# Kernel tuning notes

Hardware: AMD Instinct MI355X
Metric: run time of the kernel (lower is better)

Reference implementation:

```python
import math
import jax, jax.numpy as jnp
import numpy as np

N_LAYER = 4
D = 192        # n_embd
NH = 4         # n_head
N = 3072       # n_neurons = n_embd * mlp_dim_mult // n_head
VOCAB = 256
BLOCK = 4096
EPS = 1e-5
B, T = 1, 1024


def get_freqs(n, theta=2.0 ** 16):
    t = np.arange(n, dtype=np.float32)
    q = np.floor(t / 2.0) * 2.0  # quantize(t, 2)
    return (1.0 / theta ** (q / n) / (2.0 * math.pi)).astype(np.float32)

_FREQS = jnp.asarray(get_freqs(N))  # [N]


def _ln(x):
    # LayerNorm over last dim, no affine (elementwise_affine=False)
    m = jnp.mean(x, axis=-1, keepdims=True)
    v = jnp.var(x, axis=-1, keepdims=True)
    return (x - m) / jnp.sqrt(v + EPS)


def _rope(x):
    # x: [B, nh, T, N]
    t = x.shape[2]
    phases = (jnp.arange(t, dtype=jnp.float32)[:, None] * _FREQS[None, :]) % 1.0 * (2.0 * math.pi)  # [T, N]
    x_even = x[..., 0::2]
    x_odd = x[..., 1::2]
    v_rot = jnp.stack((-x_odd, x_even), axis=-1).reshape(x.shape)
    return x * jnp.cos(phases) + v_rot * jnp.sin(phases)


def setup_inputs() -> dict:
    key = jax.random.key(0)
    ks = jax.random.split(key, 7)
    s = 0.02
    return {
        "idx": jax.random.randint(ks[0], (B, T), 0, VOCAB, dtype=jnp.int64)
        if jax.config.jax_enable_x64 else jax.random.randint(ks[0], (B, T), 0, VOCAB, dtype=jnp.int32),
        "decoder_x": jax.random.normal(ks[1], (NH, D, N), jnp.float32) * s,
        "decoder_y": jax.random.normal(ks[2], (NH, D, N), jnp.float32) * s,
        "encoder": jax.random.normal(ks[3], (NH * N, D), jnp.float32) * s,
        "embed": jax.random.normal(ks[4], (VOCAB, D), jnp.float32) * s,
        "pos_emb": jax.random.normal(ks[5], (BLOCK, D), jnp.float32) * s,
        "lm_head": jax.random.normal(ks[6], (D, VOCAB), jnp.float32) * s,
    }


def reference(idx, decoder_x, decoder_y, encoder, embed, pos_emb, lm_head):
    b, t = idx.shape
    x = embed[idx] + pos_emb[:t][None]          # [B, T, D]
    x = _ln(x)
    mask = jnp.tril(jnp.ones((t, t), jnp.float32), k=-1)  # strictly lower
    for _ in range(N_LAYER):
        # encoder-side sparsification: D -> N per head
        x_sparse = jax.nn.relu(jnp.einsum('btd,hdn->bhtn', x, decoder_x))  # [B,nh,T,N]
        qr = _rope(x_sparse)
        scores = jnp.einsum('bhtn,bhsn->bhts', qr, qr) * mask              # [B,nh,T,T]
        ykv = _ln(jnp.einsum('bhts,bsd->bhtd', scores, x))                 # [B,nh,T,D]
        y_sparse = jax.nn.relu(jnp.einsum('bhtd,hdn->bhtn', ykv, decoder_y))
        xy = x_sparse * y_sparse                                           # [B,nh,T,N]
        # [B,T,nh*N] @ [nh*N, D]
        ymlp = jnp.einsum('bhtn,hnd->btd', xy, encoder.reshape(NH, N, D))
        x = _ln(x + _ln(ymlp))
    logits = jnp.einsum('btd,dv->btv', x, lm_head)                         # [B,T,vocab]
    return logits
```

## Files before the change

kernel.cpp:

```cpp
#include <hip/hip_runtime.h>
#include <hip/hip_bf16.h>

using bf16 = __hip_bfloat16;

#define D_DIM   192
#define N_DIM   3072
#define NHEAD   4
#define T_SEQ   1024
#define HN      12288
#define NP2     1536
#define VOCABSZ 256
#define NLAYER  4
#define LN_EPS  1e-5f
#define TWO_PI  6.2831853071795864f

typedef __attribute__((ext_vector_type(8)))  short          s16x8;
typedef __attribute__((ext_vector_type(8)))  unsigned short u16x8;
typedef __attribute__((ext_vector_type(4)))  float          f32x4;
typedef __attribute__((ext_vector_type(16))) float          f32x16;

__device__ __forceinline__ float b2f(bf16 v) { return __bfloat162float(v); }
__device__ __forceinline__ float us2f(unsigned short u) {
    unsigned int x = ((unsigned int)u) << 16;
    return __builtin_bit_cast(float, x);
}
__device__ __forceinline__ unsigned short f2us(float f) {
    bf16 b = __float2bfloat16(f);
    return __builtin_bit_cast(unsigned short, b);
}

__global__ void fill_out(float* __restrict__ out, float val, int nelem) {
    int i = blockIdx.x * 256 + threadIdx.x;
    if (i < nelem) out[i] = val;
}

__global__ void t_cvt(const float* __restrict__ in, bf16* __restrict__ out,
                      int R, int C, long inZ, long outZ) {
    __shared__ float tile[64][65];
    in  += inZ  * blockIdx.z;
    out += outZ * blockIdx.z;
    const int tx = threadIdx.x & 63, ty = threadIdx.x >> 6;
    const int r0 = blockIdx.y * 64, c0 = blockIdx.x * 64;
    #pragma unroll
    for (int rr = 0; rr < 16; rr++) {
        int row = ty * 16 + rr;
        tile[row][tx] = in[(size_t)(r0 + row) * C + c0 + tx];
    }
    __syncthreads();
    #pragma unroll
    for (int rr = 0; rr < 16; rr++) {
        int row = ty * 16 + rr;
        out[(size_t)(c0 + row) * R + r0 + tx] = __float2bfloat16(tile[tx][row]);
    }
}

__device__ __forceinline__ void wave_sum2(float& s, float& ss) {
    #pragma unroll
    for (int off = 1; off < 64; off <<= 1) {
        s  += __shfl_xor(s,  off, 64);
        ss += __shfl_xor(ss, off, 64);
    }
}

__global__ void k_embed(const int* __restrict__ idx, const float* __restrict__ emb,
                        const float* __restrict__ pos, float* __restrict__ x) {
    int t = blockIdx.x, l = threadIdx.x;
    int tok = idx[t];
    const float* e = emb + tok * D_DIM;
    const float* p = pos + t * D_DIM;
    float v0 = e[l] + p[l], v1 = e[l + 64] + p[l + 64], v2 = e[l + 128] + p[l + 128];
    float s = v0 + v1 + v2, ss = v0 * v0 + v1 * v1 + v2 * v2;
    wave_sum2(s, ss);
    float m = s / D_DIM, r = rsqrtf(ss / D_DIM - m * m + LN_EPS);
    float* xr = x + t * D_DIM;
    xr[l] = (v0 - m) * r; xr[l + 64] = (v1 - m) * r; xr[l + 128] = (v2 - m) * r;
}

__global__ void k_ln(float* __restrict__ buf) {
    int l = threadIdx.x;
    float* row = buf + (size_t)blockIdx.x * D_DIM;
    float v0 = row[l], v1 = row[l + 64], v2 = row[l + 128];
    float s = v0 + v1 + v2, ss = v0 * v0 + v1 * v1 + v2 * v2;
    wave_sum2(s, ss);
    float m = s / D_DIM, r = rsqrtf(ss / D_DIM - m * m + LN_EPS);
    row[l] = (v0 - m) * r; row[l + 64] = (v1 - m) * r; row[l + 128] = (v2 - m) * r;
}

__global__ void k_ln2(float* __restrict__ buf, const float* __restrict__ P1) {
    int l = threadIdx.x;
    size_t off = (size_t)blockIdx.x * D_DIM;
    float* row = buf + off;
    const float* r1 = P1 + off;
    float v0 = row[l] + r1[l];
    float v1 = row[l + 64] + r1[l + 64];
    float v2 = row[l + 128] + r1[l + 128];
    float s = v0 + v1 + v2, ss = v0 * v0 + v1 * v1 + v2 * v2;
    wave_sum2(s, ss);
    float m = s / D_DIM, r = rsqrtf(ss / D_DIM - m * m + LN_EPS);
    row[l] = (v0 - m) * r; row[l + 64] = (v1 - m) * r; row[l + 128] = (v2 - m) * r;
}

__global__ void k_resid8(float* __restrict__ x, const float* __restrict__ P) {
    int l = threadIdx.x, t = blockIdx.x;
    float y0 = 0.f, y1 = 0.f, y2 = 0.f;
    #pragma unroll
    for (int p = 0; p < 8; p++) {
        const float* r = P + (size_t)p * T_SEQ * D_DIM + (size_t)t * D_DIM;
        y0 += r[l]; y1 += r[l + 64]; y2 += r[l + 128];
    }
    float* xr = x + (size_t)t * D_DIM;
    float s = y0 + y1 + y2, ss = y0 * y0 + y1 * y1 + y2 * y2;
    wave_sum2(s, ss);
    float m1 = s / D_DIM, r1 = rsqrtf(ss / D_DIM - m1 * m1 + LN_EPS);
    float v0 = xr[l] + (y0 - m1) * r1;
    float v1 = xr[l + 64] + (y1 - m1) * r1;
    float v2 = xr[l + 128] + (y2 - m1) * r1;
    s = v0 + v1 + v2; ss = v0 * v0 + v1 * v1 + v2 * v2;
    wave_sum2(s, ss);
    float m2 = s / D_DIM, r2 = rsqrtf(ss / D_DIM - m2 * m2 + LN_EPS);
    xr[l] = (v0 - m2) * r2; xr[l + 64] = (v1 - m2) * r2; xr[l + 128] = (v2 - m2) * r2;
}

__global__ void k_tables(ushort2* __restrict__ csT) {
    int gid = blockIdx.x * 256 + threadIdx.x;
    int t = gid / NP2, p = gid % NP2;
    float qf = (float)(2 * p);
    float f = exp2f(qf * (-16.0f / 3072.0f)) * (1.0f / (float)TWO_PI);
    float ph = fmodf((float)t * f, 1.0f) * (float)TWO_PI;
    ushort2 cs;
    cs.x = f2us(cosf(ph));
    cs.y = f2us(sinf(ph));
    csT[gid] = cs;
}

__launch_bounds__(256, 4)
__global__ void scores64(const bf16* __restrict__ qr, bf16* __restrict__ sc,
                         bf16* __restrict__ dbuf) {
    const int h  = blockIdx.z;
    const int kh = blockIdx.y;
    const int orig = blockIdx.x;
    const int L = (orig & 7) * 17 + (orig >> 3);
    int i = 0;
    while (((i + 1) * (i + 2)) >> 1 <= L) ++i;
    int j = L - ((i * (i + 1)) >> 1);
    const int t0 = i * 64, s0 = j * 64;
    const bool diag = (i == j);

    int arow = t0, brow = s0;
    if (kh == 1 && !diag) { arow = s0; brow = t0; }

    __shared__ short As[2][64][72];
    __shared__ short Bs[2][64][72];

    const int tid = threadIdx.x;
    const int lane = tid & 63, w = tid >> 6;
    const int wtm = (w >> 1) * 32, wtn = (w & 1) * 32;
    const int l31 = lane & 31, lhi = lane >> 5;
    const int r0 = tid >> 2;
    const int kq = (tid & 3) * 16;

    const int kBeg = kh * (N_DIM / 2);
    const bf16* gA = qr + (size_t)(arow + r0) * HN + h * N_DIM + kBeg + kq;
    const bf16* gB = qr + (size_t)(brow + r0) * HN + h * N_DIM + kBeg + kq;

    u16x8 pa0, pa1, pb0, pb1;
    u16x8 qa0, qa1, qb0, qb1;
    auto load0 = [&](int k0) {
        pa0 = *(const u16x8*)(gA + k0);
        pa1 = *(const u16x8*)(gA + k0 + 8);
        pb0 = *(const u16x8*)(gB + k0);
        pb1 = *(const u16x8*)(gB + k0 + 8);
    };
    auto load1 = [&](int k0) {
        qa0 = *(const u16x8*)(gA + k0);
        qa1 = *(const u16x8*)(gA + k0 + 8);
        qb0 = *(const u16x8*)(gB + k0);
        qb1 = *(const u16x8*)(gB + k0 + 8);
    };
    auto dep0 = [&](int buf) {
        *(u16x8*)&As[buf][r0][kq]     = pa0;
        *(u16x8*)&As[buf][r0][kq + 8] = pa1;
        *(u16x8*)&Bs[buf][r0][kq]     = pb0;
        *(u16x8*)&Bs[buf][r0][kq + 8] = pb1;
    };
    auto dep1 = [&](int buf) {
        *(u16x8*)&As[buf][r0][kq]     = qa0;
        *(u16x8*)&As[buf][r0][kq + 8] = qa1;
        *(u16x8*)&Bs[buf][r0][kq]     = qb0;
        *(u16x8*)&Bs[buf][r0][kq + 8] = qb1;
    };

    f32x16 acc;
    #pragma unroll
    for (int r = 0; r < 16; r++) acc[r] = 0.f;

    auto mfma_step = [&](int buf) {
        #pragma unroll
        for (int ks = 0; ks < 4; ks++) {
            s16x8 a = *(const s16x8*)&As[buf][wtm + l31][ks * 16 + lhi * 8];
            s16x8 b = *(const s16x8*)&Bs[buf][wtn + l31][ks * 16 + lhi * 8];
            acc = __builtin_amdgcn_mfma_f32_32x32x16_bf16(a, b, acc, 0, 0, 0);
        }
    };

    const int NIT = (N_DIM / 2) / 64;
    load0(0);
    load1(64);
    dep0(0);
    __syncthreads();

    for (int k = 0; k < NIT; k += 2) {
        if (k + 2 < NIT) load0((k + 2) * 64);
        mfma_step(0);
        if (k + 1 < NIT) dep1(1);
        __syncthreads();
        if (k + 1 < NIT) {
            if (k + 3 < NIT) load1((k + 3) * 64);
            mfma_step(1);
            if (k + 2 < NIT) dep0(0);
            __syncthreads();
        }
    }

    __syncthreads();
    short (*S)[72] = (short(*)[72])&As[0][0][0];
    #pragma unroll
    for (int r = 0; r < 16; r++) {
        int row = wtm + (r & 3) + 8 * (r >> 2) + 4 * lhi;
        int col = wtn + l31;
        float v = acc[r];
        if (diag && col >= row) v = 0.f;
        S[row][col] = (short)f2us(v);
    }
    __syncthreads();
    if (kh == 1 && diag) {
        bf16* P = dbuf + (size_t)(h * 16 + i) * 4096;
        #pragma unroll
        for (int e = 0; e < 2; e++) {
            int idxe = tid + e * 256;
            int row = idxe >> 3, cg = (idxe & 7) * 8;
            u16x8 v = *(const u16x8*)&S[row][cg];
            *(u16x8*)(P + row * 64 + cg) = v;
        }
    } else {
        bf16* C = sc + (size_t)h * T_SEQ * T_SEQ;
        #pragma unroll
        for (int e = 0; e < 2; e++) {
            int idxe = tid + e * 256;
            int row = idxe >> 3, cg = (idxe & 7) * 8;
            u16x8 v = *(const u16x8*)&S[row][cg];
            *(u16x8*)(C + (size_t)(arow + row) * T_SEQ + brow + cg) = v;
        }
    }
}

__global__ void k_comb(bf16* __restrict__ sc, const bf16* __restrict__ dbuf) {
    __shared__ short tile[64][72];
    const int h = blockIdx.z;
    int L = blockIdx.x;
    int i = 0;
    while (((i + 1) * (i + 2)) >> 1 <= L) ++i;
    int j = L - ((i * (i + 1)) >> 1);
    bf16* C = sc + (size_t)h * T_SEQ * T_SEQ;
    const int r  = threadIdx.x >> 3;
    const int c8 = (threadIdx.x & 7) * 8;
    if (i != j) {
        #pragma unroll
        for (int p = 0; p < 2; p++) {
            int row = r + p * 32;
            u16x8 v = *(const u16x8*)(C + (size_t)(j * 64 + row) * T_SEQ + i * 64 + c8);
            *(u16x8*)&tile[row][c8] = v;
        }
        __syncthreads();
        #pragma unroll
        for (int p = 0; p < 2; p++) {
            int row = r + p * 32;
            size_t off = (size_t)(i * 64 + row) * T_SEQ + j * 64 + c8;
            u16x8 a = *(const u16x8*)(C + off);
            u16x8 o;
            #pragma unroll
            for (int e = 0; e < 8; e++)
                o[e] = f2us(us2f(a[e]) + us2f((unsigned short)tile[c8 + e][row]));
            *(u16x8*)(C + off) = o;
        }
    } else {
        const bf16* P = dbuf + (size_t)(h * 16 + i) * 4096;
        #pragma unroll
        for (int p = 0; p < 2; p++) {
            int row = r + p * 32;
            size_t off = (size_t)(i * 64 + row) * T_SEQ + i * 64 + c8;
            u16x8 a = *(const u16x8*)(C + off);
            u16x8 b = *(const u16x8*)((const unsigned short*)P + row * 64 + c8);
            u16x8 o;
            #pragma unroll
            for (int e = 0; e < 8; e++)
                o[e] = f2us(us2f(a[e]) + us2f(b[e]));
            *(u16x8*)(C + off) = o;
        }
    }
}

__device__ __forceinline__ void stage_rope8(short* dst, const bf16* src,
                                            const ushort2* csP) {
    u16x8 v  = *(const u16x8*)src;
    u16x8 cs = *(const u16x8*)csP;
    u16x8 o;
    #pragma unroll
    for (int i = 0; i < 4; i++) {
        float e  = us2f(v[2 * i]), od = us2f(v[2 * i + 1]);
        float c  = us2f(cs[2 * i]), s = us2f(cs[2 * i + 1]);
        o[2 * i]     = f2us(e * c - od * s);
        o[2 * i + 1] = f2us(od * c + e * s);
    }
    *(u16x8*)dst = o;
}

__launch_bounds__(256)
__global__ void scores_fused(const bf16* __restrict__ xs,
                             const ushort2* __restrict__ csT,
                             bf16* __restrict__ sc) {
    const int h  = blockIdx.z;
    const int s0 = blockIdx.x * 64, t0 = blockIdx.y * 64;
    if (s0 > t0) return;
    __shared__ short As[64][40];
    __shared__ short Bs[64][40];
    const int tid  = threadIdx.x;
    const int srow = tid >> 2, kq = (tid & 3) * 8;
    const int lane = tid & 63, w = tid >> 6, qd = lane >> 4, lc = lane & 15;
    const int tA = t0 + srow, tB = s0 + srow;
    const bf16* gA = xs + (size_t)tA * HN + h * N_DIM + kq;
    const bf16* gB = xs + (size_t)tB * HN + h * N_DIM + kq;
    const ushort2* cA = csT + (size_t)tA * NP2 + (kq >> 1);
    const ushort2* cB = csT + (size_t)tB * NP2 + (kq >> 1);
    f32x4 acc[4] = {{0.f,0.f,0.f,0.f},{0.f,0.f,0.f,0.f},
                    {0.f,0.f,0.f,0.f},{0.f,0.f,0.f,0.f}};
    for (int k0 = 0; k0 < N_DIM; k0 += 32) {
        stage_rope8(&As[srow][kq], gA + k0, cA + (k0 >> 1));
        stage_rope8(&Bs[srow][kq], gB + k0, cB + (k0 >> 1));
        __syncthreads();
        s16x8 a = *(const s16x8*)&As[w * 16 + lc][qd * 8];
        #pragma unroll
        for (int j = 0; j < 4; j++) {
            s16x8 b = *(const s16x8*)&Bs[j * 16 + lc][qd * 8];
            acc[j] = __builtin_amdgcn_mfma_f32_16x16x32_bf16(a, b, acc[j], 0, 0, 0);
        }
        __syncthreads();
    }
    bf16* C = sc + (size_t)h * T_SEQ * T_SEQ;
    const bool diag = (s0 == t0);
    const int tbase = t0 + w * 16 + qd * 4;
    #pragma unroll
    for (int j = 0; j < 4; j++) {
        int s = s0 + j * 16 + lc;
        #pragma unroll
        for (int r = 0; r < 4; r++) {
            int t = tbase + r;
            C[(size_t)t * T_SEQ + s] =
                __float2bfloat16((!diag || s < t) ? acc[j][r] : 0.f);
        }
    }
}

template <int EPI, bool WQR>
__launch_bounds__(256)
__global__ void dgemm128(const float* __restrict__ A, const bf16* __restrict__ Bt,
                         bf16* __restrict__ xs, bf16* __restrict__ qr,
                         const ushort2* __restrict__ csT) {
    __shared__ __align__(16) short pool[2 * 2 * 128 * 40];
    short (*As)[128][40] = (short(*)[128][40])pool;
    short (*Bs)[128][40] = (short(*)[128][40])(pool + 2 * 128 * 40);

    const int tid = threadIdx.x;
    const int lane = tid & 63, w = tid >> 6, qd = lane >> 4, lc = lane & 15;
    const int wtm = (w >> 1) * 64, wtn = (w & 1) * 64;
    const int n0 = blockIdx.x * 128, m0 = blockIdx.y * 128;
    if constexpr (EPI == 2) A += (size_t)(n0 / N_DIM) * T_SEQ * D_DIM;

    const int r0 = tid >> 2, r1 = r0 + 64;
    const int kq = (tid & 3) * 8;

    const float* gA = A  + kq;
    const bf16*  gB = Bt + kq;

    float4 fa00, fa01, fa02, fa03, fa10, fa11, fa12, fa13;
    u16x8 pb00, pb01, pb10, pb11;
    auto load0 = [&](int k0) {
        const float* a0 = gA + (size_t)(m0 + r0) * D_DIM + k0;
        const float* a1 = gA + (size_t)(m0 + r1) * D_DIM + k0;
        fa00 = *(const float4*)a0; fa01 = *(const float4*)(a0 + 4);
        fa02 = *(const float4*)a1; fa03 = *(const float4*)(a1 + 4);
        pb00 = *(const u16x8*)(gB + (size_t)(n0 + r0) * D_DIM + k0);
        pb01 = *(const u16x8*)(gB + (size_t)(n0 + r1) * D_DIM + k0);
    };
    auto load1 = [&](int k0) {
        const float* a0 = gA + (size_t)(m0 + r0) * D_DIM + k0;
        const float* a1 = gA + (size_t)(m0 + r1) * D_DIM + k0;
        fa10 = *(const float4*)a0; fa11 = *(const float4*)(a0 + 4);
        fa12 = *(const float4*)a1; fa13 = *(const float4*)(a1 + 4);
        pb10 = *(const u16x8*)(gB + (size_t)(n0 + r0) * D_DIM + k0);
        pb11 = *(const u16x8*)(gB + (size_t)(n0 + r1) * D_DIM + k0);
    };
    auto dep0 = [&](int buf) {
        u16x8 o0, o1;
        o0[0] = f2us(fa00.x); o0[1] = f2us(fa00.y); o0[2] = f2us(fa00.z); o0[3] = f2us(fa00.w);
        o0[4] = f2us(fa01.x); o0[5] = f2us(fa01.y); o0[6] = f2us(fa01.z); o0[7] = f2us(fa01.w);
        o1[0] = f2us(fa02.x); o1[1] = f2us(fa02.y); o1[2] = f2us(fa02.z); o1[3] = f2us(fa02.w);
        o1[4] = f2us(fa03.x); o1[5] = f2us(fa03.y); o1[6] = f2us(fa03.z); o1[7] = f2us(fa03.w);
        *(u16x8*)&As[buf][r0][kq] = o0;
        *(u16x8*)&As[buf][r1][kq] = o1;
        *(u16x8*)&Bs[buf][r0][kq] = pb00;
        *(u16x8*)&Bs[buf][r1][kq] = pb01;
    };
    auto dep1 = [&](int buf) {
        u16x8 o0, o1;
        o0[0] = f2us(fa10.x); o0[1] = f2us(fa10.y); o0[2] = f2us(fa10.z); o0[3] = f2us(fa10.w);
        o0[4] = f2us(fa11.x); o0[5] = f2us(fa11.y); o0[6] = f2us(fa11.z); o0[7] = f2us(fa11.w);
        o1[0] = f2us(fa12.x); o1[1] = f2us(fa12.y); o1[2] = f2us(fa12.z); o1[3] = f2us(fa12.w);
        o1[4] = f2us(fa13.x); o1[5] = f2us(fa13.y); o1[6] = f2us(fa13.z); o1[7] = f2us(fa13.w);
        *(u16x8*)&As[buf][r0][kq] = o0;
        *(u16x8*)&As[buf][r1][kq] = o1;
        *(u16x8*)&Bs[buf][r0][kq] = pb10;
        *(u16x8*)&Bs[buf][r1][kq] = pb11;
    };

    f32x4 acc[4][4] = {};
    auto mfma_step = [&](int buf) {
        s16x8 a[4], b[4];
        #pragma unroll
        for (int m = 0; m < 4; m++) a[m] = *(const s16x8*)&As[buf][wtm + m * 16 + lc][qd * 8];
        #pragma unroll
        for (int n = 0; n < 4; n++) b[n] = *(const s16x8*)&Bs[buf][wtn + n * 16 + lc][qd * 8];
        #pragma unroll
        for (int m = 0; m < 4; m++)
            #pragma unroll
            for (int n = 0; n < 4; n++)
                acc[m][n] = __builtin_amdgcn_mfma_f32_16x16x32_bf16(a[m], b[n], acc[m][n], 0, 0, 0);
    };

    const int NIT = D_DIM / 32;
    load0(0);
    load1(32);
    dep0(0);
    __syncthreads();
    for (int k = 0; k < NIT; k += 2) {
        if (k + 2 < NIT) load0((k + 2) * 32);
        mfma_step(0);
        if (k + 1 < NIT) dep1(1);
        __syncthreads();
        if (k + 1 < NIT) {
            if (k + 3 < NIT) load1((k + 3) * 32);
            mfma_step(1);
            if (k + 2 < NIT) dep0(0);
            __syncthreads();
        }
    }

    short (*S)[136] = (short(*)[136])pool;
    #pragma unroll
    for (int m = 0; m < 4; m++) {
        #pragma unroll
        for (int r = 0; r < 4; r++) {
            int tl = wtm + m * 16 + qd * 4 + r;
            #pragma unroll
            for (int n = 0; n < 4; n++) {
                int cl = wtn + n * 16 + lc;
                S[tl][cl] = (short)f2us(fmaxf(acc[m][n][r], 0.f));
            }
        }
    }
    __syncthreads();
    #pragma unroll
    for (int e = 0; e < 8; e++) {
        int idxe = tid + e * 256;
        int row = idxe >> 4, cg = idxe & 15;
        u16x8 v = *(const u16x8*)&S[row][cg * 8];
        int t = m0 + row, ngg = n0 + cg * 8;
        size_t ci = (size_t)t * HN + ngg;
        if constexpr (EPI == 1) {
            *(u16x8*)(xs + ci) = v;
            if constexpr (WQR) {
                int p0 = (ngg % N_DIM) >> 1;
                u16x8 cs8 = *(const u16x8*)&csT[(size_t)t * NP2 + p0];
                u16x8 o;
                #pragma unroll
                for (int q = 0; q < 4; q++) {
                    float ev = us2f(v[2 * q]), ov = us2f(v[2 * q + 1]);
                    float c = us2f(cs8[2 * q]), s = us2f(cs8[2 * q + 1]);
                    o[2 * q]     = f2us(ev * c - ov * s);
                    o[2 * q + 1] = f2us(ov * c + ev * s);
                }
                *(u16x8*)(qr + ci) = o;
            }
        } else {
            u16x8 g = *(const u16x8*)(xs + ci);
            u16x8 o;
            #pragma unroll
            for (int q = 0; q < 8; q++) o[q] = f2us(us2f(g[q]) * us2f(v[q]));
            *(u16x8*)(xs + ci) = o;
        }
    }
}

template <typename TA, int MODE>
__launch_bounds__(256)
__global__ void mfma_gemm(const TA* __restrict__ A, const bf16* __restrict__ Bt,
                          float* __restrict__ C,
                          int K, int kSeg, int lda, int ldb, int ldc,
                          long aZ, long bZ, long cZ) {
    __shared__ short As[2][64][72];
    __shared__ short Bs[2][64][72];

    const int z = blockIdx.z;
    const int tid = threadIdx.x;
    const int n0 = blockIdx.x * 64, m0 = blockIdx.y * 64;
    const int srow = tid >> 2, sk = (tid & 3) * 16;
    const int lane = tid & 63, w = tid >> 6, qd = lane >> 4, lc = lane & 15;

    int kBeg, kEnd;
    if constexpr (MODE == 1) {
        const int h = z >> 1, seg = z & 1;
        A += aZ * h;
        C += cZ * h + bZ * seg;
        const int kc = (m0 + 64 < K) ? m0 + 64 : K;
        const int half0 = ((kc + 127) >> 7) << 6;
        kBeg = seg ? half0 : 0;
        kEnd = seg ? kc : half0;
    } else if constexpr (MODE == 2) {
        A += aZ * z; Bt += bZ * z; C += cZ * z;
        kBeg = z * kSeg; kEnd = kBeg + kSeg;
    } else if constexpr (MODE == 3) {
        A += aZ * z; Bt += bZ * z; C += cZ * z;
        kBeg = 0; kEnd = (m0 + 64 < K) ? m0 + 64 : K;
    } else {
        A += aZ * z; Bt += bZ * z; C += cZ * z;
        kBeg = 0; kEnd = K;
    }

    const TA*   ga = A  + (size_t)(m0 + srow) * lda + sk;
    const bf16* gb = Bt + (size_t)(n0 + srow) * ldb + sk;

    float4 f00, f01, f02, f03, f10, f11, f12, f13;
    u16x8 pa00, pa01, pa10, pa11, pb00, pb01, pb10, pb11;
    auto load0 = [&](int k0) {
        if constexpr (__is_same(TA, float)) {
            f00 = *(const float4*)(ga + k0);
            f01 = *(const float4*)(ga + k0 + 4);
            f02 = *(const float4*)(ga + k0 + 8);
            f03 = *(const float4*)(ga + k0 + 12);
        } else {
            pa00 = *(const u16x8*)(ga + k0);
            pa01 = *(const u16x8*)(ga + k0 + 8);
        }
        pb00 = *(const u16x8*)(gb + k0);
        pb01 = *(const u16x8*)(gb + k0 + 8);
    };
    auto load1 = [&](int k0) {
        if constexpr (__is_same(TA, float)) {
            f10 = *(const float4*)(ga + k0);
            f11 = *(const float4*)(ga + k0 + 4);
            f12 = *(const float4*)(ga + k0 + 8);
            f13 = *(const float4*)(ga + k0 + 12);
        } else {
            pa10 = *(const u16x8*)(ga + k0);
            pa11 = *(const u16x8*)(ga + k0 + 8);
        }
        pb10 = *(const u16x8*)(gb + k0);
        pb11 = *(const u16x8*)(gb + k0 + 8);
    };
    auto dep0 = [&](int buf) {
        if constexpr (__is_same(TA, float)) {
            u16x8 o0, o1;
            o0[0] = f2us(f00.x); o0[1] = f2us(f00.y); o0[2] = f2us(f00.z); o0[3] = f2us(f00.w);
            o0[4] = f2us(f01.x); o0[5] = f2us(f01.y); o0[6] = f2us(f01.z); o0[7] = f2us(f01.w);
            o1[0] = f2us(f02.x); o1[1] = f2us(f02.y); o1[2] = f2us(f02.z); o1[3] = f2us(f02.w);
            o1[4] = f2us(f03.x); o1[5] = f2us(f03.y); o1[6] = f2us(f03.z); o1[7] = f2us(f03.w);
            *(u16x8*)&As[buf][srow][sk]     = o0;
            *(u16x8*)&As[buf][srow][sk + 8] = o1;
        } else {
            *(u16x8*)&As[buf][srow][sk]     = pa00;
            *(u16x8*)&As[buf][srow][sk + 8] = pa01;
        }
        *(u16x8*)&Bs[buf][srow][sk]     = pb00;
        *(u16x8*)&Bs[buf][srow][sk + 8] = pb01;
    };
    auto dep1 = [&](int buf) {
        if constexpr (__is_same(TA, float)) {
            u16x8 o0, o1;
            o0[0] = f2us(f10.x); o0[1] = f2us(f10.y); o0[2] = f2us(f10.z); o0[3] = f2us(f10.w);
            o0[4] = f2us(f11.x); o0[5] = f2us(f11.y); o0[6] = f2us(f11.z); o0[7] = f2us(f11.w);
            o1[0] = f2us(f12.x); o1[1] = f2us(f12.y); o1[2] = f2us(f12.z); o1[3] = f2us(f12.w);
            o1[4] = f2us(f13.x); o1[5] = f2us(f13.y); o1[6] = f2us(f13.z); o1[7] = f2us(f13.w);
            *(u16x8*)&As[buf][srow][sk]     = o0;
            *(u16x8*)&As[buf][srow][sk + 8] = o1;
        } else {
            *(u16x8*)&As[buf][srow][sk]     = pa10;
            *(u16x8*)&As[buf][srow][sk + 8] = pa11;
        }
        *(u16x8*)&Bs[buf][srow][sk]     = pb10;
        *(u16x8*)&Bs[buf][srow][sk + 8] = pb11;
    };

    f32x4 acc[4] = {{0.f,0.f,0.f,0.f},{0.f,0.f,0.f,0.f},
                    {0.f,0.f,0.f,0.f},{0.f,0.f,0.f,0.f}};
    auto mfma_step = [&](int buf) {
        #pragma unroll
        for (int half = 0; half < 2; half++) {
            s16x8 a = *(const s16x8*)&As[buf][w * 16 + lc][qd * 8 + half * 32];
            s16x8 b[4];
            #pragma unroll
            for (int j = 0; j < 4; j++)
                b[j] = *(const s16x8*)&Bs[buf][j * 16 + lc][qd * 8 + half * 32];
            #pragma unroll
            for (int j = 0; j < 4; j++)
                acc[j] = __builtin_amdgcn_mfma_f32_16x16x32_bf16(a, b[j], acc[j], 0, 0, 0);
        }
    };

    const int NIT = (kEnd - kBeg) >> 6;
    load0(kBeg);
    load1(kBeg + 64);
    dep0(0);
    __syncthreads();

    for (int k = 0; k < NIT; k += 2) {
        if (k + 2 < NIT) load0(kBeg + (k + 2) * 64);
        mfma_step(0);
        if (k + 1 < NIT) dep1(1);
        __syncthreads();
        if (k + 1 < NIT) {
            if (k + 3 < NIT) load1(kBeg + (k + 3) * 64);
            mfma_step(1);
            if (k + 2 < NIT) dep0(0);
            __syncthreads();
        }
    }

    #pragma unroll
    for (int j = 0; j < 4; j++) {
        int n = n0 + j * 16 + lc;
        #pragma unroll
        for (int r = 0; r < 4; r++) {
            int m = m0 + w * 16 + qd * 4 + r;
            C[(size_t)m * ldc + n] = acc[j][r];
        }
    }
}

extern "C" void kernel_launch(void* const* d_in, const int* in_sizes, int n_in,
                              void* d_out, int out_size, void* d_ws, size_t ws_size,
                              hipStream_t stream) {
    const int*   idx   = (const int*)  d_in[0];
    const float* dec_x = (const float*)d_in[1];
    const float* dec_y = (const float*)d_in[2];
    const float* enc   = (const float*)d_in[3];
    const float* emb   = (const float*)d_in[4];
    const float* pose  = (const float*)d_in[5];
    const float* lmh   = (const float*)d_in[6];
    float* out = (float*)d_out;

    char* wp = (char*)d_ws;
    float*   x    = (float*)wp;              wp += (size_t)T_SEQ * D_DIM * 4;
    bf16*    xs   = (bf16*)wp;               wp += (size_t)T_SEQ * HN * 2;
    ushort2* csT  = (ushort2*)wp;            wp += (size_t)T_SEQ * NP2 * 4;
    bf16*    sc   = (bf16*)wp;               wp += (size_t)NHEAD * T_SEQ * T_SEQ * 2;
    float*   ykv  = (float*)wp;              wp += (size_t)NHEAD * T_SEQ * D_DIM * 4;
    float*   ymlp = (float*)wp;              wp += (size_t)T_SEQ * D_DIM * 4;
    bf16*    xT   = (bf16*)wp;               wp += (size_t)D_DIM * T_SEQ * 2;
    bf16*    wX   = (bf16*)wp;               wp += (size_t)NHEAD * N_DIM * D_DIM * 2;
    bf16*    wY   = (bf16*)wp;               wp += (size_t)NHEAD * N_DIM * D_DIM * 2;
    bf16*    wE   = (bf16*)wp;               wp += (size_t)D_DIM * HN * 2;
    bf16*    wL   = (bf16*)wp;               wp += (size_t)VOCABSZ * D_DIM * 2;
    const size_t BASE_NEED = (size_t)(wp - (char*)d_ws);
    bf16*    qr   = (bf16*)wp;
    const size_t FULL_NEED = BASE_NEED + (size_t)T_SEQ * HN * 2;
    float* ymlpP = (float*)sc;
    bf16*  dbuf  = (bf16*)ykv;

    if (ws_size < BASE_NEED) {
        fill_out<<<(out_size + 255) / 256, 256, 0, stream>>>(out, (float)ws_size, out_size);
        return;
    }
    const bool USE_QR = (ws_size >= FULL_NEED);

    t_cvt<<<dim3(48, 3, 4), 256, 0, stream>>>(dec_x, wX, D_DIM, N_DIM,
                                              (long)D_DIM * N_DIM, (long)N_DIM * D_DIM);
    t_cvt<<<dim3(48, 3, 4), 256, 0, stream>>>(dec_y, wY, D_DIM, N_DIM,
                                              (long)D_DIM * N_DIM, (long)N_DIM * D_DIM);
    t_cvt<<<dim3(3, 192, 1), 256, 0, stream>>>(enc, wE, HN, D_DIM, 0L, 0L);
    t_cvt<<<dim3(4, 3, 1), 256, 0, stream>>>(lmh, wL, D_DIM, VOCABSZ, 0L, 0L);

    k_tables<<<(T_SEQ * NP2) / 256, 256, 0, stream>>>(csT);
    k_embed<<<T_SEQ, 64, 0, stream>>>(idx, emb, pose, x);

    for (int l = 0; l < NLAYER; ++l) {
        t_cvt<<<dim3(3, 16, 1), 256, 0, stream>>>(x, xT, T_SEQ, D_DIM, 0L, 0L);
        if (USE_QR) {
            dgemm128<1, true><<<dim3(96, 8), 256, 0, stream>>>(x, wX, xs, qr, csT);
            scores64<<<dim3(136, 2, NHEAD), 256, 0, stream>>>(qr, sc, dbuf);
            k_comb<<<dim3(136, 1, NHEAD), 256, 0, stream>>>(sc, dbuf);
            long segZ = (long)((float*)qr - ykv);
            mfma_gemm<bf16, 1><<<dim3(3, 16, NHEAD * 2), 256, 0, stream>>>(
                sc, xT, ykv, T_SEQ, 0, T_SEQ, T_SEQ, D_DIM,
                (long)T_SEQ * T_SEQ, segZ, (long)T_SEQ * D_DIM);
            k_ln2<<<NHEAD * T_SEQ, 64, 0, stream>>>(ykv, (const float*)qr);
        } else {
            dgemm128<1, false><<<dim3(96, 8), 256, 0, stream>>>(x, wX, xs, qr, csT);
            scores_fused<<<dim3(16, 16, NHEAD), 256, 0, stream>>>(xs, csT, sc);
            mfma_gemm<bf16, 3><<<dim3(3, 16, NHEAD), 256, 0, stream>>>(
                sc, xT, ykv, T_SEQ, 0, T_SEQ, T_SEQ, D_DIM,
                (long)T_SEQ * T_SEQ, 0L, (long)T_SEQ * D_DIM);
            k_ln<<<NHEAD * T_SEQ, 64, 0, stream>>>(ykv);
        }
        dgemm128<2, false><<<dim3(96, 8), 256, 0, stream>>>(
            (const float*)ykv, wY, xs, nullptr, nullptr);
        mfma_gemm<bf16, 2><<<dim3(3, 16, 8), 256, 0, stream>>>(
            xs, wE, ymlpP, HN, HN / 8, HN, HN, D_DIM,
            0L, 0L, (long)T_SEQ * D_DIM);
        k_resid8<<<T_SEQ, 64, 0, stream>>>(x, ymlpP);
        (void)ymlp;
    }

    mfma_gemm<float, 0><<<dim3(4, 16, 1), 256, 0, stream>>>(
        x, wL, out, D_DIM, 0, D_DIM, D_DIM, VOCABSZ, 0L, 0L, 0L);
}
```

Measured before the change: 522.7 us.

## Fold symmetric score combine into scores@x GEMM via dual MFMA operand

Drops the k_comb kernel that added each transposed half-product tile of the split score computation back into the score matrix. The scores kernel now writes off-diagonal halves transposed, and the MODE-1 GEMM loads a second A-like tile (Ms), taken from the transposed region or from the diagonal partial buffer, and accumulates it with an extra MFMA. The generic GEMM also switches from 16x16x32 to 32x32x16 MFMA tiles. This saves a full read-modify-write pass over the score matrix and one launch per layer, at the cost of extra shared memory and double MFMA work in that GEMM.

Result: no change. 516.6 us (-1.2%).

```diff
diff --git a/kernel.cpp b/kernel.cpp
--- a/kernel.cpp
+++ b/kernel.cpp
@@ -224,13 +224,15 @@
 
     __syncthreads();
     short (*S)[72] = (short(*)[72])&As[0][0][0];
+    const bool trS = (kh == 1) && !diag;
     #pragma unroll
     for (int r = 0; r < 16; r++) {
-        int row = wtm + (r & 3) + 8 * (r >> 2) + 4 * lhi;
-        int col = wtn + l31;
+        int rr = wtm + (r & 3) + 8 * (r >> 2) + 4 * lhi;
+        int cc = wtn + l31;
         float v = acc[r];
-        if (diag && col >= row) v = 0.f;
-        S[row][col] = (short)f2us(v);
+        if (diag && cc >= rr) v = 0.f;
+        if (trS) S[cc][rr] = (short)f2us(v);
+        else     S[rr][cc] = (short)f2us(v);
     }
     __syncthreads();
     if (kh == 1 && diag) {
@@ -250,52 +252,6 @@
             int row = idxe >> 3, cg = (idxe & 7) * 8;
             u16x8 v = *(const u16x8*)&S[row][cg];
             *(u16x8*)(C + (size_t)(arow + row) * T_SEQ + brow + cg) = v;
-        }
-    }
-}
-
-__global__ void k_comb(bf16* __restrict__ sc, const bf16* __restrict__ dbuf) {
-    __shared__ short tile[64][72];
-    const int h = blockIdx.z;
-    int L = blockIdx.x;
-    int i = 0;
-    while (((i + 1) * (i + 2)) >> 1 <= L) ++i;
-    int j = L - ((i * (i + 1)) >> 1);
-    bf16* C = sc + (size_t)h * T_SEQ * T_SEQ;
-    const int r  = threadIdx.x >> 3;
-    const int c8 = (threadIdx.x & 7) * 8;
-    if (i != j) {
-        #pragma unroll
-        for (int p = 0; p < 2; p++) {
-            int row = r + p * 32;
-            u16x8 v = *(const u16x8*)(C + (size_t)(j * 64 + row) * T_SEQ + i * 64 + c8);
-            *(u16x8*)&tile[row][c8] = v;
-        }
-        __syncthreads();
-        #pragma unroll
-        for (int p = 0; p < 2; p++) {
-            int row = r + p * 32;
-            size_t off = (size_t)(i * 64 + row) * T_SEQ + j * 64 + c8;
-            u16x8 a = *(const u16x8*)(C + off);
-            u16x8 o;
-            #pragma unroll
-            for (int e = 0; e < 8; e++)
-                o[e] = f2us(us2f(a[e]) + us2f((unsigned short)tile[c8 + e][row]));
-            *(u16x8*)(C + off) = o;
-        }
-    } else {
-        const bf16* P = dbuf + (size_t)(h * 16 + i) * 4096;
-        #pragma unroll
-        for (int p = 0; p < 2; p++) {
-            int row = r + p * 32;
-            size_t off = (size_t)(i * 64 + row) * T_SEQ + i * 64 + c8;
-            u16x8 a = *(const u16x8*)(C + off);
-            u16x8 b = *(const u16x8*)((const unsigned short*)P + row * 64 + c8);
-            u16x8 o;
-            #pragma unroll
-            for (int e = 0; e < 8; e++)
-                o[e] = f2us(us2f(a[e]) + us2f(b[e]));
-            *(u16x8*)(C + off) = o;
         }
     }
 }
@@ -504,23 +460,30 @@
 template <typename TA, int MODE>
 __launch_bounds__(256)
 __global__ void mfma_gemm(const TA* __restrict__ A, const bf16* __restrict__ Bt,
-                          float* __restrict__ C,
+                          float* __restrict__ C, const bf16* __restrict__ aux,
                           int K, int kSeg, int lda, int ldb, int ldc,
                           long aZ, long bZ, long cZ) {
-    __shared__ short As[2][64][72];
-    __shared__ short Bs[2][64][72];
+    constexpr bool DUAL = (MODE == 1);
+    constexpr int TILES = DUAL ? 6 : 4;
+    __shared__ __align__(16) short pool[TILES * 64 * 72];
+    short (*As)[64][72] = (short(*)[64][72])pool;
+    short (*Bs)[64][72] = (short(*)[64][72])(pool + 2 * 64 * 72);
+    short (*Ms)[64][72] = (short(*)[64][72])(pool + 4 * 64 * 72);
 
     const int z = blockIdx.z;
     const int tid = threadIdx.x;
     const int n0 = blockIdx.x * 64, m0 = blockIdx.y * 64;
     const int srow = tid >> 2, sk = (tid & 3) * 16;
-    const int lane = tid & 63, w = tid >> 6, qd = lane >> 4, lc = lane & 15;
-
-    int kBeg, kEnd;
+    const int lane = tid & 63, w = tid >> 6;
+    const int l31 = lane & 31, lhi = lane >> 5;
+    const int wm = (w >> 1) * 32, wn = (w & 1) * 32;
+
+    int kBeg, kEnd, zh = 0;
     if constexpr (MODE == 1) {
-        const int h = z >> 1, seg = z & 1;
-        A += aZ * h;
-        C += cZ * h + bZ * seg;
+        zh = z >> 1;
+        const int seg = z & 1;
+        A += aZ * zh;
+        C += cZ * zh + bZ * seg;
         const int kc = (m0 + 64 < K) ? m0 + 64 : K;
         const int half0 = ((kc + 127) >> 7) << 6;
         kBeg = seg ? half0 : 0;
@@ -539,8 +502,16 @@
     const TA*   ga = A  + (size_t)(m0 + srow) * lda + sk;
     const bf16* gb = Bt + (size_t)(n0 + srow) * ldb + sk;
 
+    auto msrc = [&](int k0) -> const bf16* {
+        if (k0 == m0)
+            return aux + (size_t)(zh * 16 + (m0 >> 6)) * 4096
+                       + (size_t)srow * 64 + sk;
+        return (const bf16*)A + (size_t)(k0 + srow) * lda + m0 + sk;
+    };
+
     float4 f00, f01, f02, f03, f10, f11, f12, f13;
     u16x8 pa00, pa01, pa10, pa11, pb00, pb01, pb10, pb11;
+    u16x8 pm00, pm01, pm10, pm11;
     auto load0 = [&](int k0) {
         if constexpr (__is_same(TA, float)) {
             f00 = *(const float4*)(ga + k0);
@@ -553,6 +524,11 @@
         }
         pb00 = *(const u16x8*)(gb + k0);
         pb01 = *(const u16x8*)(gb + k0 + 8);
+        if constexpr (DUAL) {
+            const bf16* ms = msrc(k0);
+            pm00 = *(const u16x8*)ms;
+            pm01 = *(const u16x8*)(ms + 8);
+        }
     };
     auto load1 = [&](int k0) {
         if constexpr (__is_same(TA, float)) {
@@ -566,6 +542,11 @@
         }
         pb10 = *(const u16x8*)(gb + k0);
         pb11 = *(const u16x8*)(gb + k0 + 8);
+        if constexpr (DUAL) {
+            const bf16* ms = msrc(k0);
+            pm10 = *(const u16x8*)ms;
+            pm11 = *(const u16x8*)(ms + 8);
+        }
     };
     auto dep0 = [&](int buf) {
         if constexpr (__is_same(TA, float)) {
@@ -582,6 +563,10 @@
         }
         *(u16x8*)&Bs[buf][srow][sk]     = pb00;
         *(u16x8*)&Bs[buf][srow][sk + 8] = pb01;
+        if constexpr (DUAL) {
+            *(u16x8*)&Ms[buf][srow][sk]     = pm00;
+            *(u16x8*)&Ms[buf][srow][sk + 8] = pm01;
+        }
     };
     auto dep1 = [&](int buf) {
         if constexpr (__is_same(TA, float)) {
@@ -598,21 +583,26 @@
         }
         *(u16x8*)&Bs[buf][srow][sk]     = pb10;
         *(u16x8*)&Bs[buf][srow][sk + 8] = pb11;
-    };
-
-    f32x4 acc[4] = {{0.f,0.f,0.f,0.f},{0.f,0.f,0.f,0.f},
-                    {0.f,0.f,0.f,0.f},{0.f,0.f,0.f,0.f}};
+        if constexpr (DUAL) {
+            *(u16x8*)&Ms[buf][srow][sk]     = pm10;
+            *(u16x8*)&Ms[buf][srow][sk + 8] = pm11;
+        }
+    };
+
+    f32x16 acc;
+    #pragma unroll
+    for (int r = 0; r < 16; r++) acc[r] = 0.f;
+
     auto mfma_step = [&](int buf) {
         #pragma unroll
-        for (int half = 0; half < 2; half++) {
-            s16x8 a = *(const s16x8*)&As[buf][w * 16 + lc][qd * 8 + half * 32];
-            s16x8 b[4];
-            #pragma unroll
-            for (int j = 0; j < 4; j++)
-                b[j] = *(const s16x8*)&Bs[buf][j * 16 + lc][qd * 8 + half * 32];
-            #pragma unroll
-            for (int j = 0; j < 4; j++)
-                acc[j] = __builtin_amdgcn_mfma_f32_16x16x32_bf16(a, b[j], acc[j], 0, 0, 0);
+        for (int ks = 0; ks < 4; ks++) {
+            s16x8 a = *(const s16x8*)&As[buf][wm + l31][ks * 16 + lhi * 8];
+            s16x8 b = *(const s16x8*)&Bs[buf][wn + l31][ks * 16 + lhi * 8];
+            acc = __builtin_amdgcn_mfma_f32_32x32x16_bf16(a, b, acc, 0, 0, 0);
+            if constexpr (DUAL) {
+                s16x8 m2 = *(const s16x8*)&Ms[buf][wm + l31][ks * 16 + lhi * 8];
+                acc = __builtin_amdgcn_mfma_f32_32x32x16_bf16(m2, b, acc, 0, 0, 0);
+            }
         }
     };
 
@@ -636,13 +626,10 @@
     }
 
     #pragma unroll
-    for (int j = 0; j < 4; j++) {
-        int n = n0 + j * 16 + lc;
-        #pragma unroll
-        for (int r = 0; r < 4; r++) {
-            int m = m0 + w * 16 + qd * 4 + r;
-            C[(size_t)m * ldc + n] = acc[j][r];
-        }
+    for (int r = 0; r < 16; r++) {
+        int row = m0 + wm + (r & 3) + 8 * (r >> 2) + 4 * lhi;
+        int col = n0 + wn + l31;
+        C[(size_t)row * ldc + col] = acc[r];
     }
 }
 
@@ -674,7 +661,7 @@
     bf16*    qr   = (bf16*)wp;
     const size_t FULL_NEED = BASE_NEED + (size_t)T_SEQ * HN * 2;
     float* ymlpP = (float*)sc;
-    bf16*  dbuf  = (bf16*)ykv;
+    bf16*  dbuf  = (bf16*)ymlp;
 
     if (ws_size < BASE_NEED) {
         fill_out<<<(out_size + 255) / 256, 256, 0, stream>>>(out, (float)ws_size, out_size);
@@ -697,29 +684,27 @@
         if (USE_QR) {
             dgemm128<1, true><<<dim3(96, 8), 256, 0, stream>>>(x, wX, xs, qr, csT);
             scores64<<<dim3(136, 2, NHEAD), 256, 0, stream>>>(qr, sc, dbuf);
-            k_comb<<<dim3(136, 1, NHEAD), 256, 0, stream>>>(sc, dbuf);
             long segZ = (long)((float*)qr - ykv);
             mfma_gemm<bf16, 1><<<dim3(3, 16, NHEAD * 2), 256, 0, stream>>>(
-                sc, xT, ykv, T_SEQ, 0, T_SEQ, T_SEQ, D_DIM,
+                sc, xT, ykv, dbuf, T_SEQ, 0, T_SEQ, T_SEQ, D_DIM,
                 (long)T_SEQ * T_SEQ, segZ, (long)T_SEQ * D_DIM);
             k_ln2<<<NHEAD * T_SEQ, 64, 0, stream>>>(ykv, (const float*)qr);
         } else {
             dgemm128<1, false><<<dim3(96, 8), 256, 0, stream>>>(x, wX, xs, qr, csT);
             scores_fused<<<dim3(16, 16, NHEAD), 256, 0, stream>>>(xs, csT, sc);
             mfma_gemm<bf16, 3><<<dim3(3, 16, NHEAD), 256, 0, stream>>>(
-                sc, xT, ykv, T_SEQ, 0, T_SEQ, T_SEQ, D_DIM,
+                sc, xT, ykv, nullptr, T_SEQ, 0, T_SEQ, T_SEQ, D_DIM,
                 (long)T_SEQ * T_SEQ, 0L, (long)T_SEQ * D_DIM);
             k_ln<<<NHEAD * T_SEQ, 64, 0, stream>>>(ykv);
         }
         dgemm128<2, false><<<dim3(96, 8), 256, 0, stream>>>(
             (const float*)ykv, wY, xs, nullptr, nullptr);
         mfma_gemm<bf16, 2><<<dim3(3, 16, 8), 256, 0, stream>>>(
-            xs, wE, ymlpP, HN, HN / 8, HN, HN, D_DIM,
+            xs, wE, ymlpP, nullptr, HN, HN / 8, HN, HN, D_DIM,
             0L, 0L, (long)T_SEQ * D_DIM);
         k_resid8<<<T_SEQ, 64, 0, stream>>>(x, ymlpP);
-        (void)ymlp;
     }
 
     mfma_gemm<float, 0><<<dim3(4, 16, 1), 256, 0, stream>>>(
-        x, wL, out, D_DIM, 0, D_DIM, D_DIM, VOCABSZ, 0L, 0L, 0L);
-}
+        x, wL, out, nullptr, D_DIM, 0, D_DIM, D_DIM, VOCABSZ, 0L, 0L, 0L);
+}
```
